# Performance work log

Measured on AMD Instinct MI355X. Metric: run time of the kernel, lower is better.

Reference implementation:

```python
import jax, jax.numpy as jnp
import numpy as np
from jax.ops import segment_sum

IN_DIM, HID_DIM, OUT_DIM = 128, 128, 64
N_NODES, N_EDGES = 50000, 800000


def gcn_conv(x, src, dst, W, b, n_nodes):
    # Symmetric GCN normalization (no self loops): deg at targets from unit weights
    deg = segment_sum(jnp.ones(src.shape[0], dtype=x.dtype), dst, num_segments=n_nodes)
    dinv = jnp.where(deg > 0, jax.lax.rsqrt(jnp.maximum(deg, 1.0)), 0.0)
    norm = dinv[src] * dinv[dst]                      # [E]
    h = x @ W                                         # [N, out] small GEMM first (PyG order)
    msg = h[src] * norm[:, None]                      # gather + scale: [E, out]
    out = segment_sum(msg, dst, num_segments=n_nodes) # scatter-add to targets
    return out + b


def setup_inputs() -> dict:
    key = jax.random.key(0)
    k1, k2, k3, k4, k5 = jax.random.split(key, 5)
    x = jax.random.normal(k1, (N_NODES, IN_DIM), dtype=jnp.float32)
    edge_index = jax.random.randint(k2, (2, N_EDGES), 0, N_NODES, dtype=jnp.int64)
    s1 = 1.0 / np.sqrt(IN_DIM)
    s2 = 1.0 / np.sqrt(HID_DIM)
    W1 = jax.random.uniform(k3, (IN_DIM, HID_DIM), jnp.float32, -s1, s1)
    b1 = jnp.zeros((HID_DIM,), jnp.float32)
    W2 = jax.random.uniform(k4, (HID_DIM, OUT_DIM), jnp.float32, -s2, s2)
    b2 = jnp.zeros((OUT_DIM,), jnp.float32)
    return {"x": x, "edge_index": edge_index, "W1": W1, "b1": b1, "W2": W2, "b2": b2}


def reference(x, edge_index, W1, b1, W2, b2):
    n_nodes = x.shape[0]
    src, dst = edge_index[0], edge_index[1]
    h = gcn_conv(x, src, dst, W1, b1, n_nodes)
    h = jax.nn.relu(h)
    # Dropout is identity in eval mode (reference is deterministic)
    out = gcn_conv(h, src, dst, W2, b2, n_nodes)
    return out
```

## Files before the change

kernel.cpp:

```cpp
#include <hip/hip_runtime.h>

#define N_NODES 50000
#define N_EDGES 800000
#define IN_DIM  128
#define HID_DIM 128
#define OUT_DIM 64

#define NPAD 50176
#define NB 7
#define KEYS (N_NODES * NB)
#define KPAD 350208
#define NB_SCAN2 (KPAD / 1024)
#define FILLB ((N_EDGES / 4 + 255) / 256)
#define GEMM1B ((N_NODES + 63) / 64)
#define DINVB ((N_NODES + 1023) / 1024)

typedef __attribute__((ext_vector_type(8))) short bf16x8;
typedef __attribute__((ext_vector_type(4))) float f32x4;

__device__ __forceinline__ unsigned short f2bf(float f) {
    unsigned u = __float_as_uint(f);
    u += 0x7fffu + ((u >> 16) & 1u);
    return (unsigned short)(u >> 16);
}
__device__ __forceinline__ float bflo(unsigned u) { return __uint_as_float(u << 16); }
__device__ __forceinline__ float bfhi(unsigned u) { return __uint_as_float(u & 0xffff0000u); }

#define ACC8(u)  do { \
    acc[0] += bflo(u.x); acc[1] += bfhi(u.x); \
    acc[2] += bflo(u.y); acc[3] += bfhi(u.y); \
    acc[4] += bflo(u.z); acc[5] += bfhi(u.z); \
    acc[6] += bflo(u.w); acc[7] += bfhi(u.w); } while (0)


__global__ void rank_hist_kernel(const int* __restrict__ src, const int* __restrict__ dst,
                                 int* __restrict__ cnt2, int* __restrict__ rank) {
    int e = blockIdx.x * 256 + threadIdx.x;
    if (e >= N_EDGES) return;
    int s = src[e], d = dst[e];
    rank[e] = atomicAdd(&cnt2[d * NB + (s >> 13)], 1);
}


__global__ __launch_bounds__(1024) void scan_all_kernel(const int* __restrict__ cnt2,
                                                        int* __restrict__ partials,
                                                        int* __restrict__ rs,
                                                        float* __restrict__ dinv,
                                                        const float* __restrict__ W1,
                                                        const float* __restrict__ W2,
                                                        unsigned short* __restrict__ w1t,
                                                        unsigned short* __restrict__ w2t) {
    int bid = blockIdx.x;
    int tid = threadIdx.x;
    if (bid < NB_SCAN2) {
        __shared__ int s[1024];
        __shared__ int p[1024];
        int i = bid * 1024 + tid;
        int v = (i < KEYS) ? cnt2[i] : 0;
        s[tid] = v;
        __syncthreads();
        for (int off = 1; off < 1024; off <<= 1) {
            int t = (tid >= off) ? s[tid - off] : 0;
            __syncthreads();
            s[tid] += t;
            __syncthreads();
        }
        if (tid == 0) atomicExch(&partials[bid], s[1023] + 1);
        if (bid == 0 && tid == 0) rs[KEYS] = N_EDGES;
        int myp = 0;
        if (tid < bid) {
            int val;
            do { val = atomicAdd(&partials[tid], 0); } while (val == 0);
            myp = val - 1;
        }
        p[tid] = myp;
        __syncthreads();
        for (int off = 512; off > 0; off >>= 1) {
            if (tid < off) p[tid] += p[tid + off];
            __syncthreads();
        }
        if (i < KEYS) rs[i] = p[0] + s[tid] - v;
    } else if (bid < NB_SCAN2 + DINVB) {
        int d = (bid - NB_SCAN2) * 1024 + tid;
        if (d < N_NODES) {
            int base = d * NB;
            int deg = cnt2[base] + cnt2[base + 1] + cnt2[base + 2] + cnt2[base + 3]
                    + cnt2[base + 4] + cnt2[base + 5] + cnt2[base + 6];
            dinv[d] = (deg > 0) ? rsqrtf((float)deg) : 0.0f;
        }
    } else if (bid < NB_SCAN2 + DINVB + 4) {
        int idx = (bid - NB_SCAN2 - DINVB) * 1024 + tid;
        int c = idx >> 5, k4 = (idx & 31) * 4;
        ushort4 o;
        o.x = f2bf(W1[(k4 + 0) * 128 + c]);
        o.y = f2bf(W1[(k4 + 1) * 128 + c]);
        o.z = f2bf(W1[(k4 + 2) * 128 + c]);
        o.w = f2bf(W1[(k4 + 3) * 128 + c]);
        *(ushort4*)(w1t + c * 128 + k4) = o;
    } else {
        int idx = (bid - NB_SCAN2 - DINVB - 4) * 1024 + tid;
        int c = idx >> 5, k4 = (idx & 31) * 4;
        ushort4 o;
        o.x = f2bf(W2[(k4 + 0) * 64 + c]);
        o.y = f2bf(W2[(k4 + 1) * 64 + c]);
        o.z = f2bf(W2[(k4 + 2) * 64 + c]);
        o.w = f2bf(W2[(k4 + 3) * 64 + c]);
        *(ushort4*)(w2t + c * 128 + k4) = o;
    }
}


__global__ __launch_bounds__(256) void fill_gemm1_kernel(const int* __restrict__ src,
                                                         const int* __restrict__ dst,
                                                         const int* __restrict__ rank,
                                                         const int* __restrict__ rs,
                                                         int* __restrict__ csr_src,
                                                         const float* __restrict__ x,
                                                         const unsigned short* __restrict__ w1t,
                                                         const float* __restrict__ dinv,
                                                         unsigned short* __restrict__ h1b) {
    int bid = blockIdx.x;
    if (bid < FILLB) {
        int e = (bid * 256 + threadIdx.x) * 4;
        if (e >= N_EDGES) return;
        int4 s4 = *(const int4*)(src + e);
        int4 d4 = *(const int4*)(dst + e);
        int4 r4 = *(const int4*)(rank + e);
        csr_src[rs[d4.x * NB + (s4.x >> 13)] + r4.x] = s4.x;
        csr_src[rs[d4.y * NB + (s4.y >> 13)] + r4.y] = s4.y;
        csr_src[rs[d4.z * NB + (s4.z >> 13)] + r4.z] = s4.z;
        csr_src[rs[d4.w * NB + (s4.w >> 13)] + r4.w] = s4.w;
        return;
    }

    int gb = bid - FILLB;
    int wave = threadIdx.x >> 6;
    int lane = threadIdx.x & 63;
    int n = lane & 15, quad = lane >> 4;
    int row0 = gb * 64 + wave * 16;

    int arow = row0 + n;
    if (arow >= N_NODES) arow = N_NODES - 1;
    const float* aptr = x + (size_t)arow * 128 + quad * 8;
    const unsigned short* bbase = w1t + (size_t)n * 128 + quad * 8;

    f32x4 acc[8];
#pragma unroll
    for (int t = 0; t < 8; ++t) acc[t] = (f32x4){0.f, 0.f, 0.f, 0.f};

#pragma unroll
    for (int w4 = 0; w4 < 4; ++w4) {
        float4 f0 = *(const float4*)(aptr + w4 * 32);
        float4 f1 = *(const float4*)(aptr + w4 * 32 + 4);
        bf16x8 af;
        af[0] = (short)f2bf(f0.x); af[1] = (short)f2bf(f0.y);
        af[2] = (short)f2bf(f0.z); af[3] = (short)f2bf(f0.w);
        af[4] = (short)f2bf(f1.x); af[5] = (short)f2bf(f1.y);
        af[6] = (short)f2bf(f1.z); af[7] = (short)f2bf(f1.w);
#pragma unroll
        for (int t = 0; t < 8; ++t) {
            bf16x8 bf = *(const bf16x8*)(bbase + (size_t)t * 2048 + w4 * 32);
            acc[t] = __builtin_amdgcn_mfma_f32_16x16x32_bf16(af, bf, acc[t], 0, 0, 0);
        }
    }

#pragma unroll
    for (int r = 0; r < 4; ++r) {
        int row = row0 + quad * 4 + r;
        if (row < N_NODES) {
            float dn = dinv[row];
            unsigned short* o = h1b + (size_t)row * 128 + n;
#pragma unroll
            for (int t = 0; t < 8; ++t) o[t * 16] = f2bf(acc[t][r] * dn);
        }
    }
}


#define A1T_STRIDE 136

__global__ __launch_bounds__(256) void agg1_gemm2_fused(const int* __restrict__ csr_src,
                                                        const int* __restrict__ rs,
                                                        const float* __restrict__ dinv,
                                                        const float* __restrict__ b1,
                                                        const unsigned short* __restrict__ h1b,
                                                        const unsigned short* __restrict__ w2t,
                                                        unsigned short* __restrict__ h2b) {
    __shared__ unsigned short a1t[16 * A1T_STRIDE];

    int node0 = blockIdx.x * 16;
    int g = threadIdx.x >> 4;
    int q = threadIdx.x & 15;
    int node = node0 + g;
    int start = rs[node * NB];
    int m = rs[node * NB + NB] - start;

    float acc[8] = {};
    int j = 0;
    for (; j + 3 < m; j += 4) {
        int s0 = csr_src[start + j];
        int s1 = csr_src[start + j + 1];
        int s2 = csr_src[start + j + 2];
        int s3 = csr_src[start + j + 3];
        uint4 u0 = ((const uint4*)(h1b + (size_t)s0 * 128))[q];
        uint4 u1 = ((const uint4*)(h1b + (size_t)s1 * 128))[q];
        uint4 u2 = ((const uint4*)(h1b + (size_t)s2 * 128))[q];
        uint4 u3 = ((const uint4*)(h1b + (size_t)s3 * 128))[q];
        ACC8(u0); ACC8(u1); ACC8(u2); ACC8(u3);
    }
    for (; j < m; ++j) {
        int s0 = csr_src[start + j];
        uint4 u0 = ((const uint4*)(h1b + (size_t)s0 * 128))[q];
        ACC8(u0);
    }

    {
        float dn = dinv[node];
        float4 bA = ((const float4*)b1)[2 * q];
        float4 bB = ((const float4*)b1)[2 * q + 1];
        ushort4 oA, oB;
        oA.x = f2bf(fmaxf(acc[0] * dn + bA.x, 0.f));
        oA.y = f2bf(fmaxf(acc[1] * dn + bA.y, 0.f));
        oA.z = f2bf(fmaxf(acc[2] * dn + bA.z, 0.f));
        oA.w = f2bf(fmaxf(acc[3] * dn + bA.w, 0.f));
        oB.x = f2bf(fmaxf(acc[4] * dn + bB.x, 0.f));
        oB.y = f2bf(fmaxf(acc[5] * dn + bB.y, 0.f));
        oB.z = f2bf(fmaxf(acc[6] * dn + bB.z, 0.f));
        oB.w = f2bf(fmaxf(acc[7] * dn + bB.w, 0.f));
        ushort4* o = (ushort4*)(a1t + g * A1T_STRIDE + q * 8);
        o[0] = oA;
        o[1] = oB;
    }
    __syncthreads();

    int wave = threadIdx.x >> 6;
    int lane = threadIdx.x & 63;
    int n = lane & 15, quad = lane >> 4;
    const unsigned short* bbase = w2t + (size_t)(wave * 16 + n) * 128 + quad * 8;
    const unsigned short* abase = a1t + (size_t)n * A1T_STRIDE + quad * 8;

    f32x4 c2 = (f32x4){0.f, 0.f, 0.f, 0.f};
#pragma unroll
    for (int w4 = 0; w4 < 4; ++w4) {
        bf16x8 af = *(const bf16x8*)(abase + w4 * 32);
        bf16x8 bf = *(const bf16x8*)(bbase + w4 * 32);
        c2 = __builtin_amdgcn_mfma_f32_16x16x32_bf16(af, bf, c2, 0, 0, 0);
    }

#pragma unroll
    for (int r = 0; r < 4; ++r) {
        int row = node0 + quad * 4 + r;
        float dn = dinv[row];
        h2b[(size_t)row * 64 + wave * 16 + n] = f2bf(c2[r] * dn);
    }
}


__global__ __launch_bounds__(256) void agg2_kernel(const int* __restrict__ csr_src,
                                                   const int* __restrict__ rs,
                                                   const float* __restrict__ dinv,
                                                   const float* __restrict__ b2,
                                                   const unsigned short* __restrict__ h2b,
                                                   float* __restrict__ out) {
    int node = blockIdx.x * 4 + (threadIdx.x >> 6);
    if (node >= N_NODES) return;
    int lane = threadIdx.x & 63;
    int grp = lane >> 3;
    int q   = lane & 7;
    int start = rs[node * NB];
    int m = rs[node * NB + NB] - start;

    float acc[8] = {};

    int j = grp;
    for (; j + 8 < m; j += 16) {
        int s0 = csr_src[start + j];
        int s1 = csr_src[start + j + 8];
        uint4 u0 = ((const uint4*)(h2b + (size_t)s0 * 64))[q];
        uint4 u1 = ((const uint4*)(h2b + (size_t)s1 * 64))[q];
        ACC8(u0); ACC8(u1);
    }
    if (j < m) {
        int s0 = csr_src[start + j];
        uint4 u0 = ((const uint4*)(h2b + (size_t)s0 * 64))[q];
        ACC8(u0);
    }

#pragma unroll
    for (int d = 8; d <= 32; d <<= 1) {
#pragma unroll
        for (int c = 0; c < 8; ++c) acc[c] += __shfl_xor(acc[c], d, 64);
    }

    if (lane < 8) {
        float dn = dinv[node];
        float4 bA = ((const float4*)b2)[2 * q];
        float4 bB = ((const float4*)b2)[2 * q + 1];
        float4 rA, rB;
        rA.x = acc[0] * dn + bA.x;
        rA.y = acc[1] * dn + bA.y;
        rA.z = acc[2] * dn + bA.z;
        rA.w = acc[3] * dn + bA.w;
        rB.x = acc[4] * dn + bB.x;
        rB.y = acc[5] * dn + bB.y;
        rB.z = acc[6] * dn + bB.z;
        rB.w = acc[7] * dn + bB.w;
        float4* o = (float4*)(out + (size_t)node * 64);
        o[2 * q] = rA;
        o[2 * q + 1] = rB;
    }
}


extern "C" void kernel_launch(void* const* d_in, const int* in_sizes, int n_in,
                              void* d_out, int out_size, void* d_ws, size_t ws_size,
                              hipStream_t stream) {
    const float* x  = (const float*)d_in[0];
    const int*   ei = (const int*)d_in[1];
    const float* W1 = (const float*)d_in[2];
    const float* b1 = (const float*)d_in[3];
    const float* W2 = (const float*)d_in[4];
    const float* b2 = (const float*)d_in[5];
    float* out = (float*)d_out;

    const int* src = ei;
    const int* dst = ei + N_EDGES;

    char* ws = (char*)d_ws;
    int*   cnt2      = (int*)ws;
    int*   partials  = cnt2 + KPAD;
    int*   rs        = partials + 512;
    float* dinv      = (float*)(rs + KPAD);
    int*   rank      = (int*)(dinv + NPAD);
    int*   csr_src   = rank + N_EDGES;
    unsigned short* h1b = (unsigned short*)(csr_src + N_EDGES);
    unsigned short* h2b = h1b + (size_t)N_NODES * HID_DIM;
    unsigned short* w1t = h2b + (size_t)N_NODES * OUT_DIM;
    unsigned short* w2t = w1t + 128 * 128;

    hipMemsetAsync(cnt2, 0, (KPAD + 512) * sizeof(int), stream);

    rank_hist_kernel<<<(N_EDGES + 255) / 256, 256, 0, stream>>>(src, dst, cnt2, rank);

    scan_all_kernel<<<NB_SCAN2 + DINVB + 6, 1024, 0, stream>>>(cnt2, partials, rs, dinv,
                                                               W1, W2, w1t, w2t);

    fill_gemm1_kernel<<<FILLB + GEMM1B, 256, 0, stream>>>(src, dst, rank, rs, csr_src,
                                                          x, w1t, dinv, h1b);

    agg1_gemm2_fused<<<N_NODES / 16, 256, 0, stream>>>(csr_src, rs, dinv, b1, h1b, w2t, h2b);

    agg2_kernel<<<(N_NODES + 3) / 4, 256, 0, stream>>>(csr_src, rs, dinv, b2, h2b, out);
}
```

Baseline: 206.0 us.

## Reschedule GEMM1 alongside scan and move source-degree scaling into aggregation

Weight transposes now run in the rank/histogram kernel. GEMM1 moves into the scan kernel so it overlaps the scan and dinv work instead of sharing a launch with the CSR fill, and it no longer depends on dinv. To make that possible, the source-side dinv scaling moves from GEMM1's epilogue into the layer-1 aggregation, which adds one dinv gather per edge. The block scan is also rewritten with wave shuffles instead of a shared-memory Hillis-Steele loop that used many barriers.

```diff
diff --git a/kernel.cpp b/kernel.cpp
--- a/kernel.cpp
+++ b/kernel.cpp
@@ -12,8 +12,10 @@
 #define KPAD 350208
 #define NB_SCAN2 (KPAD / 1024)
 #define FILLB ((N_EDGES / 4 + 255) / 256)
-#define GEMM1B ((N_NODES + 63) / 64)
 #define DINVB ((N_NODES + 1023) / 1024)
+#define GEMM1B1024 (NPAD / 256)
+#define RANKB (N_EDGES / 256)
+#define PREPB 24
 
 typedef __attribute__((ext_vector_type(8))) short bf16x8;
 typedef __attribute__((ext_vector_type(4))) float f32x4;
@@ -32,40 +34,85 @@
     acc[4] += bflo(u.z); acc[5] += bfhi(u.z); \
     acc[6] += bflo(u.w); acc[7] += bfhi(u.w); } while (0)
 
-
-__global__ void rank_hist_kernel(const int* __restrict__ src, const int* __restrict__ dst,
-                                 int* __restrict__ cnt2, int* __restrict__ rank) {
-    int e = blockIdx.x * 256 + threadIdx.x;
-    if (e >= N_EDGES) return;
-    int s = src[e], d = dst[e];
-    rank[e] = atomicAdd(&cnt2[d * NB + (s >> 13)], 1);
-}
-
-
-__global__ __launch_bounds__(1024) void scan_all_kernel(const int* __restrict__ cnt2,
-                                                        int* __restrict__ partials,
-                                                        int* __restrict__ rs,
-                                                        float* __restrict__ dinv,
+#define FMA8(u, sc_)  do { \
+    acc[0] += bflo(u.x) * (sc_); acc[1] += bfhi(u.x) * (sc_); \
+    acc[2] += bflo(u.y) * (sc_); acc[3] += bfhi(u.y) * (sc_); \
+    acc[4] += bflo(u.z) * (sc_); acc[5] += bfhi(u.z) * (sc_); \
+    acc[6] += bflo(u.w) * (sc_); acc[7] += bfhi(u.w) * (sc_); } while (0)
+
+
+__global__ __launch_bounds__(256) void prep_rank_kernel(const int* __restrict__ src,
+                                                        const int* __restrict__ dst,
+                                                        int* __restrict__ cnt2,
+                                                        int* __restrict__ rank,
                                                         const float* __restrict__ W1,
                                                         const float* __restrict__ W2,
                                                         unsigned short* __restrict__ w1t,
                                                         unsigned short* __restrict__ w2t) {
     int bid = blockIdx.x;
     int tid = threadIdx.x;
+    if (bid < 16) {
+        int idx = bid * 256 + tid;
+        int c = idx >> 5, k4 = (idx & 31) * 4;
+        ushort4 o;
+        o.x = f2bf(W1[(k4 + 0) * 128 + c]);
+        o.y = f2bf(W1[(k4 + 1) * 128 + c]);
+        o.z = f2bf(W1[(k4 + 2) * 128 + c]);
+        o.w = f2bf(W1[(k4 + 3) * 128 + c]);
+        *(ushort4*)(w1t + c * 128 + k4) = o;
+    } else if (bid < PREPB) {
+        int idx = (bid - 16) * 256 + tid;
+        int c = idx >> 5, k4 = (idx & 31) * 4;
+        ushort4 o;
+        o.x = f2bf(W2[(k4 + 0) * 64 + c]);
+        o.y = f2bf(W2[(k4 + 1) * 64 + c]);
+        o.z = f2bf(W2[(k4 + 2) * 64 + c]);
+        o.w = f2bf(W2[(k4 + 3) * 64 + c]);
+        *(ushort4*)(w2t + c * 128 + k4) = o;
+    } else {
+        int e = (bid - PREPB) * 256 + tid;
+        int s = src[e], d = dst[e];
+        rank[e] = atomicAdd(&cnt2[d * NB + (s >> 13)], 1);
+    }
+}
+
+
+__global__ __launch_bounds__(1024) void scan_dinv_gemm1_kernel(const int* __restrict__ cnt2,
+                                                               int* __restrict__ partials,
+                                                               int* __restrict__ rs,
+                                                               float* __restrict__ dinv,
+                                                               const float* __restrict__ x,
+                                                               const unsigned short* __restrict__ w1t,
+                                                               unsigned short* __restrict__ h1b) {
+    int bid = blockIdx.x;
+    int tid = threadIdx.x;
     if (bid < NB_SCAN2) {
-        __shared__ int s[1024];
-        __shared__ int p[1024];
+        __shared__ int wsum[16];
+        __shared__ int woffE[16];
+        __shared__ int psum[16];
+        __shared__ int bpre;
+        int lane = tid & 63, wid = tid >> 6;
         int i = bid * 1024 + tid;
         int v = (i < KEYS) ? cnt2[i] : 0;
-        s[tid] = v;
+        int s = v;
+#pragma unroll
+        for (int off = 1; off < 64; off <<= 1) {
+            int t = __shfl_up(s, off, 64);
+            if (lane >= off) s += t;
+        }
+        if (lane == 63) wsum[wid] = s;
         __syncthreads();
-        for (int off = 1; off < 1024; off <<= 1) {
-            int t = (tid >= off) ? s[tid - off] : 0;
-            __syncthreads();
-            s[tid] += t;
-            __syncthreads();
-        }
-        if (tid == 0) atomicExch(&partials[bid], s[1023] + 1);
+        if (wid == 0) {
+            int ws = (lane < 16) ? wsum[lane] : 0;
+            int wi = ws;
+#pragma unroll
+            for (int off = 1; off < 16; off <<= 1) {
+                int t = __shfl_up(wi, off, 64);
+                if (lane >= off) wi += t;
+            }
+            if (lane < 16) woffE[lane] = wi - ws;
+            if (lane == 15) atomicExch(&partials[bid], wi + 1);
+        }
         if (bid == 0 && tid == 0) rs[KEYS] = N_EDGES;
         int myp = 0;
         if (tid < bid) {
@@ -73,13 +120,18 @@
             do { val = atomicAdd(&partials[tid], 0); } while (val == 0);
             myp = val - 1;
         }
-        p[tid] = myp;
+#pragma unroll
+        for (int d = 1; d < 64; d <<= 1) myp += __shfl_xor(myp, d, 64);
+        if (lane == 0) psum[wid] = myp;
         __syncthreads();
-        for (int off = 512; off > 0; off >>= 1) {
-            if (tid < off) p[tid] += p[tid + off];
-            __syncthreads();
-        }
-        if (i < KEYS) rs[i] = p[0] + s[tid] - v;
+        if (tid == 0) {
+            int b = 0;
+#pragma unroll
+            for (int t = 0; t < 16; ++t) b += psum[t];
+            bpre = b;
+        }
+        __syncthreads();
+        if (i < KEYS) rs[i] = bpre + woffE[wid] + s - v;
     } else if (bid < NB_SCAN2 + DINVB) {
         int d = (bid - NB_SCAN2) * 1024 + tid;
         if (d < N_NODES) {
@@ -88,92 +140,65 @@
                     + cnt2[base + 4] + cnt2[base + 5] + cnt2[base + 6];
             dinv[d] = (deg > 0) ? rsqrtf((float)deg) : 0.0f;
         }
-    } else if (bid < NB_SCAN2 + DINVB + 4) {
-        int idx = (bid - NB_SCAN2 - DINVB) * 1024 + tid;
-        int c = idx >> 5, k4 = (idx & 31) * 4;
-        ushort4 o;
-        o.x = f2bf(W1[(k4 + 0) * 128 + c]);
-        o.y = f2bf(W1[(k4 + 1) * 128 + c]);
-        o.z = f2bf(W1[(k4 + 2) * 128 + c]);
-        o.w = f2bf(W1[(k4 + 3) * 128 + c]);
-        *(ushort4*)(w1t + c * 128 + k4) = o;
     } else {
-        int idx = (bid - NB_SCAN2 - DINVB - 4) * 1024 + tid;
-        int c = idx >> 5, k4 = (idx & 31) * 4;
-        ushort4 o;
-        o.x = f2bf(W2[(k4 + 0) * 64 + c]);
-        o.y = f2bf(W2[(k4 + 1) * 64 + c]);
-        o.z = f2bf(W2[(k4 + 2) * 64 + c]);
-        o.w = f2bf(W2[(k4 + 3) * 64 + c]);
-        *(ushort4*)(w2t + c * 128 + k4) = o;
-    }
-}
-
-
-__global__ __launch_bounds__(256) void fill_gemm1_kernel(const int* __restrict__ src,
-                                                         const int* __restrict__ dst,
-                                                         const int* __restrict__ rank,
-                                                         const int* __restrict__ rs,
-                                                         int* __restrict__ csr_src,
-                                                         const float* __restrict__ x,
-                                                         const unsigned short* __restrict__ w1t,
-                                                         const float* __restrict__ dinv,
-                                                         unsigned short* __restrict__ h1b) {
-    int bid = blockIdx.x;
-    if (bid < FILLB) {
-        int e = (bid * 256 + threadIdx.x) * 4;
-        if (e >= N_EDGES) return;
-        int4 s4 = *(const int4*)(src + e);
-        int4 d4 = *(const int4*)(dst + e);
-        int4 r4 = *(const int4*)(rank + e);
-        csr_src[rs[d4.x * NB + (s4.x >> 13)] + r4.x] = s4.x;
-        csr_src[rs[d4.y * NB + (s4.y >> 13)] + r4.y] = s4.y;
-        csr_src[rs[d4.z * NB + (s4.z >> 13)] + r4.z] = s4.z;
-        csr_src[rs[d4.w * NB + (s4.w >> 13)] + r4.w] = s4.w;
-        return;
-    }
-
-    int gb = bid - FILLB;
-    int wave = threadIdx.x >> 6;
-    int lane = threadIdx.x & 63;
-    int n = lane & 15, quad = lane >> 4;
-    int row0 = gb * 64 + wave * 16;
-
-    int arow = row0 + n;
-    if (arow >= N_NODES) arow = N_NODES - 1;
-    const float* aptr = x + (size_t)arow * 128 + quad * 8;
-    const unsigned short* bbase = w1t + (size_t)n * 128 + quad * 8;
-
-    f32x4 acc[8];
-#pragma unroll
-    for (int t = 0; t < 8; ++t) acc[t] = (f32x4){0.f, 0.f, 0.f, 0.f};
-
-#pragma unroll
-    for (int w4 = 0; w4 < 4; ++w4) {
-        float4 f0 = *(const float4*)(aptr + w4 * 32);
-        float4 f1 = *(const float4*)(aptr + w4 * 32 + 4);
-        bf16x8 af;
-        af[0] = (short)f2bf(f0.x); af[1] = (short)f2bf(f0.y);
-        af[2] = (short)f2bf(f0.z); af[3] = (short)f2bf(f0.w);
-        af[4] = (short)f2bf(f1.x); af[5] = (short)f2bf(f1.y);
-        af[6] = (short)f2bf(f1.z); af[7] = (short)f2bf(f1.w);
-#pragma unroll
-        for (int t = 0; t < 8; ++t) {
-            bf16x8 bf = *(const bf16x8*)(bbase + (size_t)t * 2048 + w4 * 32);
-            acc[t] = __builtin_amdgcn_mfma_f32_16x16x32_bf16(af, bf, acc[t], 0, 0, 0);
-        }
-    }
-
-#pragma unroll
-    for (int r = 0; r < 4; ++r) {
-        int row = row0 + quad * 4 + r;
-        if (row < N_NODES) {
-            float dn = dinv[row];
-            unsigned short* o = h1b + (size_t)row * 128 + n;
-#pragma unroll
-            for (int t = 0; t < 8; ++t) o[t * 16] = f2bf(acc[t][r] * dn);
-        }
-    }
+        int gb = bid - NB_SCAN2 - DINVB;
+        int wave = tid >> 6;
+        int lane = tid & 63;
+        int n = lane & 15, quad = lane >> 4;
+        int row0 = gb * 256 + wave * 16;
+
+        int arow = row0 + n;
+        if (arow >= N_NODES) arow = N_NODES - 1;
+        const float* aptr = x + (size_t)arow * 128 + quad * 8;
+        const unsigned short* bbase = w1t + (size_t)n * 128 + quad * 8;
+
+        f32x4 acc[8];
+#pragma unroll
+        for (int t = 0; t < 8; ++t) acc[t] = (f32x4){0.f, 0.f, 0.f, 0.f};
+
+#pragma unroll
+        for (int w4 = 0; w4 < 4; ++w4) {
+            float4 f0 = *(const float4*)(aptr + w4 * 32);
+            float4 f1 = *(const float4*)(aptr + w4 * 32 + 4);
+            bf16x8 af;
+            af[0] = (short)f2bf(f0.x); af[1] = (short)f2bf(f0.y);
+            af[2] = (short)f2bf(f0.z); af[3] = (short)f2bf(f0.w);
+            af[4] = (short)f2bf(f1.x); af[5] = (short)f2bf(f1.y);
+            af[6] = (short)f2bf(f1.z); af[7] = (short)f2bf(f1.w);
+#pragma unroll
+            for (int t = 0; t < 8; ++t) {
+                bf16x8 bf = *(const bf16x8*)(bbase + (size_t)t * 2048 + w4 * 32);
+                acc[t] = __builtin_amdgcn_mfma_f32_16x16x32_bf16(af, bf, acc[t], 0, 0, 0);
+            }
+        }
+
+#pragma unroll
+        for (int r = 0; r < 4; ++r) {
+            int row = row0 + quad * 4 + r;
+            if (row < N_NODES) {
+                unsigned short* o = h1b + (size_t)row * 128 + n;
+#pragma unroll
+                for (int t = 0; t < 8; ++t) o[t * 16] = f2bf(acc[t][r]);
+            }
+        }
+    }
+}
+
+
+__global__ __launch_bounds__(256) void fill_kernel(const int* __restrict__ src,
+                                                   const int* __restrict__ dst,
+                                                   const int* __restrict__ rank,
+                                                   const int* __restrict__ rs,
+                                                   int* __restrict__ csr_src) {
+    int e = (blockIdx.x * 256 + threadIdx.x) * 4;
+    if (e >= N_EDGES) return;
+    int4 s4 = *(const int4*)(src + e);
+    int4 d4 = *(const int4*)(dst + e);
+    int4 r4 = *(const int4*)(rank + e);
+    csr_src[rs[d4.x * NB + (s4.x >> 13)] + r4.x] = s4.x;
+    csr_src[rs[d4.y * NB + (s4.y >> 13)] + r4.y] = s4.y;
+    csr_src[rs[d4.z * NB + (s4.z >> 13)] + r4.z] = s4.z;
+    csr_src[rs[d4.w * NB + (s4.w >> 13)] + r4.w] = s4.w;
 }
 
 
@@ -202,16 +227,21 @@
         int s1 = csr_src[start + j + 1];
         int s2 = csr_src[start + j + 2];
         int s3 = csr_src[start + j + 3];
+        float ds0 = dinv[s0];
+        float ds1 = dinv[s1];
+        float ds2 = dinv[s2];
+        float ds3 = dinv[s3];
         uint4 u0 = ((const uint4*)(h1b + (size_t)s0 * 128))[q];
         uint4 u1 = ((const uint4*)(h1b + (size_t)s1 * 128))[q];
         uint4 u2 = ((const uint4*)(h1b + (size_t)s2 * 128))[q];
         uint4 u3 = ((const uint4*)(h1b + (size_t)s3 * 128))[q];
-        ACC8(u0); ACC8(u1); ACC8(u2); ACC8(u3);
+        FMA8(u0, ds0); FMA8(u1, ds1); FMA8(u2, ds2); FMA8(u3, ds3);
     }
     for (; j < m; ++j) {
         int s0 = csr_src[start + j];
+        float ds0 = dinv[s0];
         uint4 u0 = ((const uint4*)(h1b + (size_t)s0 * 128))[q];
-        ACC8(u0);
+        FMA8(u0, ds0);
     }
 
     {
@@ -338,15 +368,15 @@
     unsigned short* w1t = h2b + (size_t)N_NODES * OUT_DIM;
     unsigned short* w2t = w1t + 128 * 128;
 
-    hipMemsetAsync(cnt2, 0, (KPAD + 512) * sizeof(int), stream);
-
-    rank_hist_kernel<<<(N_EDGES + 255) / 256, 256, 0, stream>>>(src, dst, cnt2, rank);
-
-    scan_all_kernel<<<NB_SCAN2 + DINVB + 6, 1024, 0, stream>>>(cnt2, partials, rs, dinv,
-                                                               W1, W2, w1t, w2t);
-
-    fill_gemm1_kernel<<<FILLB + GEMM1B, 256, 0, stream>>>(src, dst, rank, rs, csr_src,
-                                                          x, w1t, dinv, h1b);
+    (void)hipMemsetAsync(cnt2, 0, (KPAD + 512) * sizeof(int), stream);
+
+    prep_rank_kernel<<<PREPB + RANKB, 256, 0, stream>>>(src, dst, cnt2, rank,
+                                                        W1, W2, w1t, w2t);
+
+    scan_dinv_gemm1_kernel<<<NB_SCAN2 + DINVB + GEMM1B1024, 1024, 0, stream>>>(
+        cnt2, partials, rs, dinv, x, w1t, h1b);
+
+    fill_kernel<<<FILLB, 256, 0, stream>>>(src, dst, rank, rs, csr_src);
 
     agg1_gemm2_fused<<<N_NODES / 16, 256, 0, stream>>>(csr_src, rs, dinv, b1, h1b, w2t, h2b);
 
```

New measurement: 212.3 us. 1.03x slower.
